# Kernel optimization log

Measured on AMD Instinct MI355X. Metric: run time of the kernel, lower is better.

The kernel has to match this reference:

```python
import jax, jax.numpy as jnp
import numpy as np

KERNEL = (3, 3)
STRIDE = (1, 1)
# padding='zero', dimPadding='auto' -> pad = ceil((k-1)/2) per side on each dim
PAD = tuple(int(np.ceil((k - 1) / 2)) for k in KERNEL)


def setup_inputs() -> dict:
    key = jax.random.key(0)
    k1, k2 = jax.random.split(key)
    dataset = jax.random.normal(k1, (32, 64, 112, 112), dtype=jnp.float32)
    filters = jax.random.normal(k2, (128, 64, 3, 3), dtype=jnp.float32)
    return {"dataset": dataset, "filters": filters}


def reference(dataset, filters):
    # The torch module's unfold->multiply->sum->fold pipeline computes a plain
    # cross-correlation (conv2d) of NCHW input with OIHW filters, zero padding
    # PAD per side, stride STRIDE. Output: [B, F, Hout, Wout].
    out = jax.lax.conv_general_dilated(
        dataset, filters,
        window_strides=STRIDE,
        padding=((PAD[0], PAD[0]), (PAD[1], PAD[1])),
        dimension_numbers=("NCHW", "OIHW", "NCHW"),
    )
    return out
```

## Files before the change

kernel.cpp:

```cpp
#include <hip/hip_runtime.h>


typedef __attribute__((ext_vector_type(8))) __bf16 bf16x8;
typedef __attribute__((ext_vector_type(4))) float f32x4;
typedef __attribute__((ext_vector_type(4))) unsigned int u32x4;

#define XROW 7296
#define WPROW 114

__device__ __forceinline__ unsigned short f2bf(float f) {
    unsigned u = __builtin_bit_cast(unsigned, f);
    u += 0x7FFF + ((u >> 16) & 1);
    return (unsigned short)(u >> 16);
}

__device__ __forceinline__ void gload_lds16(const unsigned short* g, unsigned short* l) {
    __builtin_amdgcn_global_load_lds(
        (const __attribute__((address_space(1))) unsigned int*)g,
        (__attribute__((address_space(3))) unsigned int*)l, 16, 0, 0);
}
__device__ __forceinline__ void gload_lds4(const unsigned short* g, unsigned short* l) {
    __builtin_amdgcn_global_load_lds(
        (const __attribute__((address_space(1))) unsigned int*)g,
        (__attribute__((address_space(3))) unsigned int*)l, 4, 0, 0);
}

__global__ void prep_weights(const float* __restrict__ flt,
                             unsigned short* __restrict__ wsA,
                             unsigned short* __restrict__ wsS) {
    int idx = blockIdx.x * 256 + threadIdx.x;
    if (idx >= 9 * 128 * 64) return;
    int off = idx >> 13;
    int f   = (idx >> 6) & 127;
    int c   = idx & 63;
    unsigned short v = f2bf(flt[(f * 64 + c) * 9 + off]);
    wsA[idx] = v;
    int cq = c >> 3, cl = c & 7;
    wsS[(off * 128 + f) * 64 + ((cq ^ (f & 7)) * 8 + cl)] = v;
}

__global__ __launch_bounds__(512, 4)
void prep_input(const float* __restrict__ x, unsigned short* __restrict__ xt) {
    __shared__ __align__(16) unsigned short T[112 * 64];
    const int tid  = threadIdx.x;
    const int b    = blockIdx.x / 112;
    const int h    = blockIdx.x - b * 112;
    const int li   = tid & 7;
    const int unit = tid >> 3;

    for (int it = 0; it < 2; ++it) {
        int u = it * 64 + unit;
        if (u < 112) {
            int wo = u >> 3, cq = u & 7;
            int c  = cq * 8 + li;
            const float* src = x + (((size_t)b * 64 + c) * 112 + h) * 112 + wo * 8;
            f32x4 f0 = *(const f32x4*)src;
            f32x4 f1 = *(const f32x4*)(src + 4);
            float r[8] = {f0.x, f0.y, f0.z, f0.w, f1.x, f1.y, f1.z, f1.w};
#pragma unroll
            for (int d = 1; d < 8; d <<= 1) {
#pragma unroll
                for (int jA = 0; jA < 8; ++jA) {
                    if (jA & d) continue;
                    int jB = jA | d;
                    float give = (li & d) ? r[jA] : r[jB];
                    float got  = __shfl_xor(give, d, 64);
                    if (li & d) r[jA] = got; else r[jB] = got;
                }
            }
            unsigned pk[4];
#pragma unroll
            for (int j = 0; j < 4; ++j)
                pk[j] = (unsigned)f2bf(r[2 * j]) | ((unsigned)f2bf(r[2 * j + 1]) << 16);
            int w = wo * 8 + li;
            *(u32x4*)&T[w * 64 + (cq ^ (w & 7)) * 8] = u32x4{pk[0], pk[1], pk[2], pk[3]};
        }
    }
    __syncthreads();

    unsigned short* dst = xt + ((size_t)b * 114 + (h + 1)) * XROW;
    for (int ch = tid; ch < 912; ch += 512) {
        int wp = ch >> 3, cq = ch & 7;
        u32x4 v = {0, 0, 0, 0};
        if (wp >= 1 && wp <= 112) {
            int w = wp - 1;
            v = *(const u32x4*)&T[w * 64 + (cq ^ (w & 7)) * 8];
        }
        *(u32x4*)&dst[(size_t)ch * 8] = v;
    }
    if (h == 0 || h == 111) {
        unsigned short* zr = xt + ((size_t)b * 114 + (h == 0 ? 0 : 113)) * XROW;
        for (int ch = tid; ch < 912; ch += 512)
            *(u32x4*)&zr[(size_t)ch * 8] = u32x4{0, 0, 0, 0};
    }
}

template <int TW0, int NTW>
__device__ __forceinline__ void kloop_lds(const unsigned short* Ws,
                                          const unsigned short* Bs,
                                          float* obase, int rr, int l16, int q) {
    f32x4 acc[4][NTW];
#pragma unroll
    for (int mt = 0; mt < 4; ++mt)
#pragma unroll
        for (int t = 0; t < NTW; ++t) acc[mt][t] = {0.f, 0.f, 0.f, 0.f};

    const int e = l16 & 7;
#pragma unroll
    for (int off = 0; off < 9; ++off) {
        const int kh = off / 3;
        const int kw = off - kh * 3;
        const int rp = rr + kh;
#pragma unroll
        for (int cs = 0; cs < 2; ++cs) {
            const int cq = cs * 4 + q;
            const int ca = cq ^ e;
            bf16x8 a0 = *(const bf16x8*)&Ws[(off * 64 +      l16) * 64 + ca * 8];
            bf16x8 a1 = *(const bf16x8*)&Ws[(off * 64 + 16 + l16) * 64 + ca * 8];
            bf16x8 a2 = *(const bf16x8*)&Ws[(off * 64 + 32 + l16) * 64 + ca * 8];
            bf16x8 a3 = *(const bf16x8*)&Ws[(off * 64 + 48 + l16) * 64 + ca * 8];
#pragma unroll
            for (int t = 0; t < NTW; ++t) {
                int wp = (TW0 + t) * 16 + l16 + kw;
                int cb = cq ^ (wp & 7);
                bf16x8 bv = *(const bf16x8*)&Bs[(rp * WPROW + wp) * 64 + cb * 8];
                acc[0][t] = __builtin_amdgcn_mfma_f32_16x16x32_bf16(a0, bv, acc[0][t], 0, 0, 0);
                acc[1][t] = __builtin_amdgcn_mfma_f32_16x16x32_bf16(a1, bv, acc[1][t], 0, 0, 0);
                acc[2][t] = __builtin_amdgcn_mfma_f32_16x16x32_bf16(a2, bv, acc[2][t], 0, 0, 0);
                acc[3][t] = __builtin_amdgcn_mfma_f32_16x16x32_bf16(a3, bv, acc[3][t], 0, 0, 0);
            }
        }
    }
#pragma unroll
    for (int mt = 0; mt < 4; ++mt)
#pragma unroll
        for (int t = 0; t < NTW; ++t) {
            float* o = obase + (size_t)(mt * 16) * 12544 + (TW0 + t) * 16 + l16;
#pragma unroll
            for (int r2 = 0; r2 < 4; ++r2)
                o[(size_t)r2 * 12544] = acc[mt][t][r2];
        }
}

__global__ __launch_bounds__(512, 2)
void conv_lds(const unsigned short* __restrict__ xt,
              const unsigned short* __restrict__ wsS,
              float* __restrict__ out) {
    __shared__ __align__(16) unsigned short Ws[9 * 64 * 64];
    __shared__ __align__(16) unsigned short Bs[6 * WPROW * 64];

    const int tid = threadIdx.x;
    const int id  = blockIdx.x;
    const int xcd = id & 7;
    const int s   = id >> 3;
    const int b   = s / 7;
    const int u   = s - b * 7;
    const int ix  = xcd * 7 + u;
    const int fg  = ix & 1;
    const int quad = ix >> 1;

    const int lane = tid & 63;
    const int wid  = tid >> 6;

    const unsigned short* xrow = xt + ((size_t)b * 114 + quad * 4) * XROW;
    {
        const int l3 = lane >> 3, j = lane & 7;
        for (int i = wid; i < 156; i += 8) {
            if (i < 72) {
                int off = i >> 3, k = i & 7;
                gload_lds16(wsS + off * 8192 + fg * 4096 + k * 512 + lane * 8,
                            &Ws[off * 4096 + k * 512]);
            } else {
                int i2 = i - 72;
                int rp = i2 / 14, seg = i2 - rp * 14;
                int wp = seg * 8 + l3;
                gload_lds16(xrow + (size_t)rp * XROW + wp * 64 + ((j ^ (wp & 7)) * 8),
                            &Bs[(rp * WPROW + seg * 8) * 64]);
            }
        }
        if (wid < 6) {
            int rp = wid;
            int wp = 112 + (lane >> 5);
            int cq = (lane & 31) >> 2;
            gload_lds4(xrow + (size_t)rp * XROW + wp * 64 + (cq ^ (wp & 7)) * 8 + (lane & 3) * 2,
                       &Bs[(rp * WPROW + 112) * 64]);
        }
    }
    __syncthreads();

    const int l16 = lane & 15;
    const int q   = lane >> 4;
    const int rr  = wid & 3;
    const int ws  = wid >> 2;
    const int h   = quad * 4 + rr;

    float* obase = out + (((size_t)b * 128 + fg * 64 + q * 4) * 112 + h) * 112;

    if (ws == 0) kloop_lds<0, 4>(Ws, Bs, obase, rr, l16, q);
    else         kloop_lds<4, 3>(Ws, Bs, obase, rr, l16, q);
}

#define ROWS_PER_KH 124
#define ROW_SHORTS 64

__global__ __launch_bounds__(512, 4)
void conv_mfma(const float* __restrict__ x,
               const unsigned short* __restrict__ wsA,
               float* __restrict__ out) {
    __shared__ __align__(16) unsigned short Bso[4 * ROWS_PER_KH * ROW_SHORTS];

    const int tid = threadIdx.x;
    const int id  = blockIdx.x;
    const int xcd = id & 7;
    const int s   = id >> 3;
    const int b   = s / 7;
    const int hpl = s - b * 7;
    const int hp  = xcd * 7 + hpl;
    const int h0  = hp * 2;

    if (tid < 32) {
        int kh = tid >> 3, cq = tid & 7;
        int R = kh * ROWS_PER_KH;
        int chunk = cq ^ (R & 7);
        *(u32x4*)&Bso[R * ROW_SHORTS + chunk * 8] = u32x4{0, 0, 0, 0};
    }

    const int li   = tid & 7;
    const int unit = tid >> 3;
    for (int it = 0; it < 8; ++it) {
        int u = it * 64 + unit;
        if (u < 480) {
            int wo = u >> 5;
            int rc = u & 31;
            int rp = rc >> 3;
            int cq = rc & 7;
            int hr = h0 + rp - 1;
            int c  = cq * 8 + li;
            f32x4 f0 = {0.f, 0.f, 0.f, 0.f}, f1 = {0.f, 0.f, 0.f, 0.f};
            if ((unsigned)hr < 112u && wo < 14) {
                const float* src = x + (((size_t)b * 64 + c) * 112 + hr) * 112 + wo * 8;
                f0 = *(const f32x4*)src;
                f1 = *(const f32x4*)(src + 4);
            }
            float r[8] = {f0.x, f0.y, f0.z, f0.w, f1.x, f1.y, f1.z, f1.w};
#pragma unroll
            for (int d = 1; d < 8; d <<= 1) {
#pragma unroll
                for (int jA = 0; jA < 8; ++jA) {
                    if (jA & d) continue;
                    int jB = jA | d;
                    float give = (li & d) ? r[jA] : r[jB];
                    float got  = __shfl_xor(give, d, 64);
                    if (li & d) r[jA] = got; else r[jB] = got;
                }
            }
            int R = rp * ROWS_PER_KH + wo * 8 + li + 1;
            int chunk = cq ^ (R & 7);
            unsigned pk[4];
#pragma unroll
            for (int j = 0; j < 4; ++j)
                pk[j] = (unsigned)f2bf(r[2 * j]) | ((unsigned)f2bf(r[2 * j + 1]) << 16);
            *(u32x4*)&Bso[R * ROW_SHORTS + chunk * 8] = u32x4{pk[0], pk[1], pk[2], pk[3]};
        }
    }
    __syncthreads();

    const int lane = tid & 63;
    const int wid  = tid >> 6;
    const int fg   = wid & 3;
    const int rr   = wid >> 2;
    const int q    = lane >> 4;
    const int l16  = lane & 15;
    const int h    = h0 + rr;

    f32x4 acc[2][7];
#pragma unroll
    for (int mt = 0; mt < 2; ++mt)
#pragma unroll
        for (int tw = 0; tw < 7; ++tw)
            acc[mt][tw] = {0.f, 0.f, 0.f, 0.f};

    const unsigned short* wA = wsA + (fg * 32 + l16) * 64 + q * 8;

#pragma unroll
    for (int off = 0; off < 9; ++off) {
        const int kh = off / 3;
        const int kw = off - kh * 3;
        const int Rbase = (rr + kh) * ROWS_PER_KH + kw;
#pragma unroll
        for (int cs = 0; cs < 2; ++cs) {
            bf16x8 a0 = *(const bf16x8*)(wA + off * 8192 + cs * 32);
            bf16x8 a1 = *(const bf16x8*)(wA + off * 8192 + 1024 + cs * 32);
            const int cq = cs * 4 + q;
#pragma unroll
            for (int tw = 0; tw < 7; ++tw) {
                int R = Rbase + tw * 16 + l16;
                int chunk = cq ^ (R & 7);
                bf16x8 bv = *(const bf16x8*)&Bso[R * ROW_SHORTS + chunk * 8];
                acc[0][tw] = __builtin_amdgcn_mfma_f32_16x16x32_bf16(a0, bv, acc[0][tw], 0, 0, 0);
                acc[1][tw] = __builtin_amdgcn_mfma_f32_16x16x32_bf16(a1, bv, acc[1][tw], 0, 0, 0);
            }
        }
    }

#pragma unroll
    for (int mt = 0; mt < 2; ++mt) {
#pragma unroll
        for (int tw = 0; tw < 7; ++tw) {
            int f = fg * 32 + mt * 16 + q * 4;
            int w = tw * 16 + l16;
            float* o = out + (((size_t)b * 128 + f) * 112 + h) * 112 + w;
#pragma unroll
            for (int r2 = 0; r2 < 4; ++r2)
                o[(size_t)r2 * 12544] = acc[mt][tw][r2];
        }
    }
}

extern "C" void kernel_launch(void* const* d_in, const int* in_sizes, int n_in,
                              void* d_out, int out_size, void* d_ws, size_t ws_size,
                              hipStream_t stream) {
    const float* x   = (const float*)d_in[0];
    const float* flt = (const float*)d_in[1];
    float* out = (float*)d_out;
    unsigned short* wsA = (unsigned short*)d_ws;
    unsigned short* wsS = wsA + 73728;
    unsigned short* xxt = wsA + 147456;

    hipLaunchKernelGGL(prep_weights, dim3(288), dim3(256), 0, stream, flt, wsA, wsS);

    const size_t XT_SHORTS = (size_t)32 * 114 * 114 * 64;
    const size_t need = (147456 + XT_SHORTS) * 2;
    if (ws_size >= need) {
        hipLaunchKernelGGL(prep_input, dim3(3584), dim3(512), 0, stream, x, xxt);
        hipLaunchKernelGGL(conv_lds, dim3(1792), dim3(512), 0, stream, xxt, wsS, out);
    } else {
        hipLaunchKernelGGL(conv_mfma, dim3(1792), dim3(512), 0, stream, x, wsA, out);
    }
}
```

Before: 344.8 us.

## Process 14-row strips per block with a ring buffer of input rows

The conv kernel now assigns each block a 14-row output strip instead of a 4-row quad. It keeps a 6-slot ring of padded input rows in LDS and prefetches the next rows into registers while computing the current ones. This loads the weight tile into LDS once per strip rather than per quad and removes the halo re-reads, at the cost of a grid of only 512 blocks and an extra barrier per step. The input-prep kernel also changes its thread mapping so each wave reads contiguous width segments of one channel plane, which gives more coalesced global loads.

Measured after the change: 348.0 us. About the same (+0.9%).

```diff
diff --git a/kernel.cpp b/kernel.cpp
--- a/kernel.cpp
+++ b/kernel.cpp
@@ -45,35 +45,36 @@
     const int tid  = threadIdx.x;
     const int b    = blockIdx.x / 112;
     const int h    = blockIdx.x - b * 112;
-    const int li   = tid & 7;
-    const int unit = tid >> 3;
+    const int lane = tid & 63;
+    const int wv   = tid >> 6;
+    const int cr   = lane >> 3;
+    const int wq   = lane & 7;
+    const float* plane = x + (((size_t)b * 64 + wv * 8 + cr) * 112 + h) * 112;
 
     for (int it = 0; it < 2; ++it) {
-        int u = it * 64 + unit;
-        if (u < 112) {
-            int wo = u >> 3, cq = u & 7;
-            int c  = cq * 8 + li;
-            const float* src = x + (((size_t)b * 64 + c) * 112 + h) * 112 + wo * 8;
+        int wb = it * 64;
+        if (it == 0 || wq < 6) {
+            const float* src = plane + wb + wq * 8;
             f32x4 f0 = *(const f32x4*)src;
             f32x4 f1 = *(const f32x4*)(src + 4);
             float r[8] = {f0.x, f0.y, f0.z, f0.w, f1.x, f1.y, f1.z, f1.w};
 #pragma unroll
-            for (int d = 1; d < 8; d <<= 1) {
+            for (int dd = 1; dd < 8; dd <<= 1) {
 #pragma unroll
                 for (int jA = 0; jA < 8; ++jA) {
-                    if (jA & d) continue;
-                    int jB = jA | d;
-                    float give = (li & d) ? r[jA] : r[jB];
-                    float got  = __shfl_xor(give, d, 64);
-                    if (li & d) r[jA] = got; else r[jB] = got;
+                    if (jA & dd) continue;
+                    int jB = jA | dd;
+                    float give = (cr & dd) ? r[jA] : r[jB];
+                    float got  = __shfl_xor(give, dd * 8, 64);
+                    if (cr & dd) r[jA] = got; else r[jB] = got;
                 }
             }
+            int w = wb + wq * 8 + cr;
             unsigned pk[4];
 #pragma unroll
             for (int j = 0; j < 4; ++j)
                 pk[j] = (unsigned)f2bf(r[2 * j]) | ((unsigned)f2bf(r[2 * j + 1]) << 16);
-            int w = wo * 8 + li;
-            *(u32x4*)&T[w * 64 + (cq ^ (w & 7)) * 8] = u32x4{pk[0], pk[1], pk[2], pk[3]};
+            *(u32x4*)&T[w * 64 + ((wv ^ (w & 7)) * 8)] = u32x4{pk[0], pk[1], pk[2], pk[3]};
         }
     }
     __syncthreads();
@@ -96,21 +97,23 @@
 }
 
 template <int TW0, int NTW>
-__device__ __forceinline__ void kloop_lds(const unsigned short* Ws,
-                                          const unsigned short* Bs,
-                                          float* obase, int rr, int l16, int q) {
+__device__ __forceinline__ void kloop_ring(const unsigned short* Ws,
+                                           const unsigned short* Bs,
+                                           int rb0, int rb1, int rb2,
+                                           float* obase, int l16, int q) {
     f32x4 acc[4][NTW];
 #pragma unroll
     for (int mt = 0; mt < 4; ++mt)
 #pragma unroll
         for (int t = 0; t < NTW; ++t) acc[mt][t] = {0.f, 0.f, 0.f, 0.f};
 
+    const int rbs[3] = {rb0, rb1, rb2};
     const int e = l16 & 7;
 #pragma unroll
     for (int off = 0; off < 9; ++off) {
         const int kh = off / 3;
         const int kw = off - kh * 3;
-        const int rp = rr + kh;
+        const int rb = rbs[kh];
 #pragma unroll
         for (int cs = 0; cs < 2; ++cs) {
             const int cq = cs * 4 + q;
@@ -123,7 +126,7 @@
             for (int t = 0; t < NTW; ++t) {
                 int wp = (TW0 + t) * 16 + l16 + kw;
                 int cb = cq ^ (wp & 7);
-                bf16x8 bv = *(const bf16x8*)&Bs[(rp * WPROW + wp) * 64 + cb * 8];
+                bf16x8 bv = *(const bf16x8*)&Bs[rb + wp * 64 + cb * 8];
                 acc[0][t] = __builtin_amdgcn_mfma_f32_16x16x32_bf16(a0, bv, acc[0][t], 0, 0, 0);
                 acc[1][t] = __builtin_amdgcn_mfma_f32_16x16x32_bf16(a1, bv, acc[1][t], 0, 0, 0);
                 acc[2][t] = __builtin_amdgcn_mfma_f32_16x16x32_bf16(a2, bv, acc[2][t], 0, 0, 0);
@@ -143,26 +146,27 @@
 }
 
 __global__ __launch_bounds__(512, 2)
-void conv_lds(const unsigned short* __restrict__ xt,
-              const unsigned short* __restrict__ wsS,
-              float* __restrict__ out) {
+void conv_ring(const unsigned short* __restrict__ xt,
+               const unsigned short* __restrict__ wsS,
+               float* __restrict__ out) {
     __shared__ __align__(16) unsigned short Ws[9 * 64 * 64];
     __shared__ __align__(16) unsigned short Bs[6 * WPROW * 64];
 
     const int tid = threadIdx.x;
     const int id  = blockIdx.x;
     const int xcd = id & 7;
-    const int s   = id >> 3;
-    const int b   = s / 7;
-    const int u   = s - b * 7;
-    const int ix  = xcd * 7 + u;
-    const int fg  = ix & 1;
-    const int quad = ix >> 1;
+    const int u   = id >> 3;
+    const int lin = xcd * 64 + u;
+    const int b     = lin >> 4;
+    const int fg    = (lin >> 3) & 1;
+    const int strip = lin & 7;
+    const int H0    = strip * 14;
 
     const int lane = tid & 63;
     const int wid  = tid >> 6;
 
-    const unsigned short* xrow = xt + ((size_t)b * 114 + quad * 4) * XROW;
+    const unsigned short* xb = xt + (size_t)b * 114 * XROW;
+
     {
         const int l3 = lane >> 3, j = lane & 7;
         for (int i = wid; i < 156; i += 8) {
@@ -173,17 +177,19 @@
             } else {
                 int i2 = i - 72;
                 int rp = i2 / 14, seg = i2 - rp * 14;
+                int slot = (H0 + rp) % 6;
                 int wp = seg * 8 + l3;
-                gload_lds16(xrow + (size_t)rp * XROW + wp * 64 + ((j ^ (wp & 7)) * 8),
-                            &Bs[(rp * WPROW + seg * 8) * 64]);
+                gload_lds16(xb + (size_t)(H0 + rp) * XROW + wp * 64 + ((j ^ (wp & 7)) * 8),
+                            &Bs[(slot * WPROW + seg * 8) * 64]);
             }
         }
         if (wid < 6) {
             int rp = wid;
+            int slot = (H0 + rp) % 6;
             int wp = 112 + (lane >> 5);
             int cq = (lane & 31) >> 2;
-            gload_lds4(xrow + (size_t)rp * XROW + wp * 64 + (cq ^ (wp & 7)) * 8 + (lane & 3) * 2,
-                       &Bs[(rp * WPROW + 112) * 64]);
+            gload_lds4(xb + (size_t)(H0 + rp) * XROW + wp * 64 + (cq ^ (wp & 7)) * 8 + (lane & 3) * 2,
+                       &Bs[(slot * WPROW + 112) * 64]);
         }
     }
     __syncthreads();
@@ -191,13 +197,56 @@
     const int l16 = lane & 15;
     const int q   = lane >> 4;
     const int rr  = wid & 3;
-    const int ws  = wid >> 2;
-    const int h   = quad * 4 + rr;
-
-    float* obase = out + (((size_t)b * 128 + fg * 64 + q * 4) * 112 + h) * 112;
-
-    if (ws == 0) kloop_lds<0, 4>(Ws, Bs, obase, rr, l16, q);
-    else         kloop_lds<4, 3>(Ws, Bs, obase, rr, l16, q);
+    const int wsp = wid >> 2;
+
+    for (int s = 0; s < 4; ++s) {
+        const int nrows = (s < 3) ? 4 : 2;
+        const int hs = H0 + 4 * s;
+
+        u32x4 st0[4], st1[4];
+        const int nnext = (s < 2) ? 4 : (s == 2 ? 2 : 0);
+        const int hnext = hs + 6;
+#pragma unroll
+        for (int r = 0; r < 4; ++r) {
+            if (r < nnext) {
+                const unsigned short* src = xb + (size_t)(hnext + r) * XROW;
+                st0[r] = *(const u32x4*)(src + tid * 8);
+                if (tid < 400) st1[r] = *(const u32x4*)(src + (size_t)(512 + tid) * 8);
+            }
+        }
+
+        if (rr < nrows) {
+            const int h = hs + rr;
+            int rb[3];
+#pragma unroll
+            for (int kh = 0; kh < 3; ++kh) {
+                int t = (hs % 6) + rr + kh;
+                if (t >= 6) t -= 6;
+                rb[kh] = t * (WPROW * 64);
+            }
+            float* obase = out + (((size_t)b * 128 + fg * 64 + q * 4) * 112 + h) * 112;
+            if (wsp == 0) kloop_ring<0, 4>(Ws, Bs, rb[0], rb[1], rb[2], obase, l16, q);
+            else          kloop_ring<4, 3>(Ws, Bs, rb[0], rb[1], rb[2], obase, l16, q);
+        }
+        __syncthreads();
+
+        if (s < 3) {
+#pragma unroll
+            for (int r = 0; r < 4; ++r) {
+                if (r < nnext) {
+                    int slot = (hnext + r) % 6;
+                    int wp = tid >> 3, cq = tid & 7;
+                    *(u32x4*)&Bs[(slot * WPROW + wp) * 64 + ((cq ^ (wp & 7)) * 8)] = st0[r];
+                    if (tid < 400) {
+                        int ch2 = 512 + tid;
+                        int wp2 = ch2 >> 3, cq2 = ch2 & 7;
+                        *(u32x4*)&Bs[(slot * WPROW + wp2) * 64 + ((cq2 ^ (wp2 & 7)) * 8)] = st1[r];
+                    }
+                }
+            }
+            __syncthreads();
+        }
+    }
 }
 
 #define ROWS_PER_KH 124
@@ -333,7 +382,7 @@
     const size_t need = (147456 + XT_SHORTS) * 2;
     if (ws_size >= need) {
         hipLaunchKernelGGL(prep_input, dim3(3584), dim3(512), 0, stream, x, xxt);
-        hipLaunchKernelGGL(conv_lds, dim3(1792), dim3(512), 0, stream, xxt, wsS, out);
+        hipLaunchKernelGGL(conv_ring, dim3(512), dim3(512), 0, stream, xxt, wsS, out);
     } else {
         hipLaunchKernelGGL(conv_mfma, dim3(1792), dim3(512), 0, stream, x, wsA, out);
     }
```

## Fuse weight prep into input prep, replicate weights per XCD, remap blocks

Applied to the files above, without the earlier changes.

Folds the weight conversion into the input-transpose kernel, which removes one kernel launch. Each of the 8 XCDs now gets its own copy of the swizzled weights. Block-to-(batch, row, filter-group) mapping is changed so that each XCD handles whole batches in both the prep and conv kernels, which should improve L2 locality. The input prep also changes its global read pattern so that each wave reads contiguous rows from 8 channels, and the conv kernel issues its input-tile loads before its weight loads. In exchange it uses more workspace and performs redundant weight writes.

After: 348.3 us. No clear change (+1.0%).

```diff
diff --git a/kernel.cpp b/kernel.cpp
--- a/kernel.cpp
+++ b/kernel.cpp
@@ -7,6 +7,7 @@
 
 #define XROW 7296
 #define WPROW 114
+#define WS_SHORTS 73728
 
 __device__ __forceinline__ unsigned short f2bf(float f) {
     unsigned u = __builtin_bit_cast(unsigned, f);
@@ -25,55 +26,63 @@
         (__attribute__((address_space(3))) unsigned int*)l, 4, 0, 0);
 }
 
-__global__ void prep_weights(const float* __restrict__ flt,
-                             unsigned short* __restrict__ wsA,
-                             unsigned short* __restrict__ wsS) {
-    int idx = blockIdx.x * 256 + threadIdx.x;
-    if (idx >= 9 * 128 * 64) return;
-    int off = idx >> 13;
-    int f   = (idx >> 6) & 127;
-    int c   = idx & 63;
-    unsigned short v = f2bf(flt[(f * 64 + c) * 9 + off]);
-    wsA[idx] = v;
-    int cq = c >> 3, cl = c & 7;
-    wsS[(off * 128 + f) * 64 + ((cq ^ (f & 7)) * 8 + cl)] = v;
-}
-
 __global__ __launch_bounds__(512, 4)
-void prep_input(const float* __restrict__ x, unsigned short* __restrict__ xt) {
+void prep_all(const float* __restrict__ x, const float* __restrict__ flt,
+              unsigned short* __restrict__ xt, unsigned short* __restrict__ wsS) {
     __shared__ __align__(16) unsigned short T[112 * 64];
-    const int tid  = threadIdx.x;
-    const int b    = blockIdx.x / 112;
-    const int h    = blockIdx.x - b * 112;
-    const int li   = tid & 7;
-    const int unit = tid >> 3;
+    const int tid = threadIdx.x;
+    const int bx  = blockIdx.x;
+
+    {
+        int gidx = bx * 512 + tid;
+        if (gidx < 9 * 128 * 64) {
+            int off = gidx >> 13;
+            int f   = (gidx >> 6) & 127;
+            int c   = gidx & 63;
+            unsigned short v = f2bf(flt[(f * 64 + c) * 9 + off]);
+            int cq = c >> 3, cl = c & 7;
+            size_t sidx = (size_t)(off * 128 + f) * 64 + ((cq ^ (f & 7)) * 8 + cl);
+#pragma unroll
+            for (int xc = 0; xc < 8; ++xc)
+                wsS[(size_t)xc * WS_SHORTS + sidx] = v;
+        }
+    }
+
+    const int xcd = bx & 7;
+    const int k   = bx >> 3;
+    const int b   = xcd * 4 + k / 112;
+    const int h   = k - (k / 112) * 112;
+
+    const int lane = tid & 63;
+    const int wv   = tid >> 6;
+    const int cr   = lane >> 3;
+    const int wq   = lane & 7;
+    const float* plane = x + (((size_t)b * 64 + wv * 8 + cr) * 112 + h) * 112;
 
     for (int it = 0; it < 2; ++it) {
-        int u = it * 64 + unit;
-        if (u < 112) {
-            int wo = u >> 3, cq = u & 7;
-            int c  = cq * 8 + li;
-            const float* src = x + (((size_t)b * 64 + c) * 112 + h) * 112 + wo * 8;
+        int wb = it * 64;
+        if (it == 0 || wq < 6) {
+            const float* src = plane + wb + wq * 8;
             f32x4 f0 = *(const f32x4*)src;
             f32x4 f1 = *(const f32x4*)(src + 4);
             float r[8] = {f0.x, f0.y, f0.z, f0.w, f1.x, f1.y, f1.z, f1.w};
 #pragma unroll
-            for (int d = 1; d < 8; d <<= 1) {
+            for (int dd = 1; dd < 8; dd <<= 1) {
 #pragma unroll
                 for (int jA = 0; jA < 8; ++jA) {
-                    if (jA & d) continue;
-                    int jB = jA | d;
-                    float give = (li & d) ? r[jA] : r[jB];
-                    float got  = __shfl_xor(give, d, 64);
-                    if (li & d) r[jA] = got; else r[jB] = got;
+                    if (jA & dd) continue;
+                    int jB = jA | dd;
+                    float give = (cr & dd) ? r[jA] : r[jB];
+                    float got  = __shfl_xor(give, dd * 8, 64);
+                    if (cr & dd) r[jA] = got; else r[jB] = got;
                 }
             }
+            int w = wb + wq * 8 + cr;
             unsigned pk[4];
 #pragma unroll
             for (int j = 0; j < 4; ++j)
                 pk[j] = (unsigned)f2bf(r[2 * j]) | ((unsigned)f2bf(r[2 * j + 1]) << 16);
-            int w = wo * 8 + li;
-            *(u32x4*)&T[w * 64 + (cq ^ (w & 7)) * 8] = u32x4{pk[0], pk[1], pk[2], pk[3]};
+            *(u32x4*)&T[w * 64 + ((wv ^ (w & 7)) * 8)] = u32x4{pk[0], pk[1], pk[2], pk[3]};
         }
     }
     __syncthreads();
@@ -153,30 +162,29 @@
     const int id  = blockIdx.x;
     const int xcd = id & 7;
     const int s   = id >> 3;
-    const int b   = s / 7;
-    const int u   = s - b * 7;
-    const int ix  = xcd * 7 + u;
-    const int fg  = ix & 1;
-    const int quad = ix >> 1;
+    const int b   = xcd * 4 + s / 56;
+    const int rem = s - (s / 56) * 56;
+    const int fg  = rem / 28;
+    const int quad = rem - fg * 28;
 
     const int lane = tid & 63;
     const int wid  = tid >> 6;
 
-    const unsigned short* xrow = xt + ((size_t)b * 114 + quad * 4) * XROW;
+    const unsigned short* xrow  = xt + ((size_t)b * 114 + quad * 4) * XROW;
+    const unsigned short* wbase = wsS + (size_t)xcd * WS_SHORTS + fg * 4096;
+
     {
         const int l3 = lane >> 3, j = lane & 7;
-        for (int i = wid; i < 156; i += 8) {
-            if (i < 72) {
-                int off = i >> 3, k = i & 7;
-                gload_lds16(wsS + off * 8192 + fg * 4096 + k * 512 + lane * 8,
-                            &Ws[off * 4096 + k * 512]);
-            } else {
-                int i2 = i - 72;
-                int rp = i2 / 14, seg = i2 - rp * 14;
-                int wp = seg * 8 + l3;
-                gload_lds16(xrow + (size_t)rp * XROW + wp * 64 + ((j ^ (wp & 7)) * 8),
-                            &Bs[(rp * WPROW + seg * 8) * 64]);
-            }
+        for (int i = wid; i < 84; i += 8) {
+            int rp = i / 14, seg = i - rp * 14;
+            int wp = seg * 8 + l3;
+            gload_lds16(xrow + (size_t)rp * XROW + wp * 64 + ((j ^ (wp & 7)) * 8),
+                        &Bs[(rp * WPROW + seg * 8) * 64]);
+        }
+        for (int i = wid; i < 72; i += 8) {
+            int off = i >> 3, k2 = i & 7;
+            gload_lds16(wbase + off * 8192 + k2 * 512 + lane * 8,
+                        &Ws[off * 4096 + k2 * 512]);
         }
         if (wid < 6) {
             int rp = wid;
@@ -191,13 +199,23 @@
     const int l16 = lane & 15;
     const int q   = lane >> 4;
     const int rr  = wid & 3;
-    const int ws  = wid >> 2;
+    const int wsp = wid >> 2;
     const int h   = quad * 4 + rr;
 
     float* obase = out + (((size_t)b * 128 + fg * 64 + q * 4) * 112 + h) * 112;
 
-    if (ws == 0) kloop_lds<0, 4>(Ws, Bs, obase, rr, l16, q);
-    else         kloop_lds<4, 3>(Ws, Bs, obase, rr, l16, q);
+    if (wsp == 0) kloop_lds<0, 4>(Ws, Bs, obase, rr, l16, q);
+    else          kloop_lds<4, 3>(Ws, Bs, obase, rr, l16, q);
+}
+
+__global__ void prep_weights(const float* __restrict__ flt,
+                             unsigned short* __restrict__ wsA) {
+    int idx = blockIdx.x * 256 + threadIdx.x;
+    if (idx >= 9 * 128 * 64) return;
+    int off = idx >> 13;
+    int f   = (idx >> 6) & 127;
+    int c   = idx & 63;
+    wsA[idx] = f2bf(flt[(f * 64 + c) * 9 + off]);
 }
 
 #define ROWS_PER_KH 124
@@ -323,18 +341,18 @@
     const float* x   = (const float*)d_in[0];
     const float* flt = (const float*)d_in[1];
     float* out = (float*)d_out;
-    unsigned short* wsA = (unsigned short*)d_ws;
-    unsigned short* wsS = wsA + 73728;
-    unsigned short* xxt = wsA + 147456;
-
-    hipLaunchKernelGGL(prep_weights, dim3(288), dim3(256), 0, stream, flt, wsA, wsS);
+    unsigned short* ws  = (unsigned short*)d_ws;
+    unsigned short* wsA = ws;
+    unsigned short* wsS = ws + WS_SHORTS;
+    unsigned short* xxt = ws + WS_SHORTS * 9;
 
     const size_t XT_SHORTS = (size_t)32 * 114 * 114 * 64;
-    const size_t need = (147456 + XT_SHORTS) * 2;
+    const size_t need = ((size_t)WS_SHORTS * 9 + XT_SHORTS) * 2;
     if (ws_size >= need) {
-        hipLaunchKernelGGL(prep_input, dim3(3584), dim3(512), 0, stream, x, xxt);
+        hipLaunchKernelGGL(prep_all, dim3(3584), dim3(512), 0, stream, x, flt, xxt, wsS);
         hipLaunchKernelGGL(conv_lds, dim3(1792), dim3(512), 0, stream, xxt, wsS, out);
     } else {
+        hipLaunchKernelGGL(prep_weights, dim3(288), dim3(256), 0, stream, flt, wsA);
         hipLaunchKernelGGL(conv_mfma, dim3(1792), dim3(512), 0, stream, x, wsA, out);
     }
 }
```
